# Performance work log

Measured on AMD Instinct MI355X. Metric: run time of the kernel, lower is better.

Reference implementation:

```python
import jax, jax.numpy as jnp
import numpy as np

NUM_POINTS = 72
GAMMA = 2.0
RADIUS = 15.0
W_CLS = 1.0
W_SIM = 3.0
LW_CLS = 2.0
LW_XYTL = 0.5
LW_LIOU = 2.0
K_MAX = 64
EPS = 1e-12  # F.normalize eps


def _normalize(v):
    # F.normalize over the flattened prior axis: v / max(||v||_2, eps)
    return v / jnp.maximum(jnp.linalg.norm(v), EPS)


def _liou_loss(pred, tgt):
    # pred: [..., P], tgt broadcastable; line IoU with radius, loss = 1 - iou
    lo = jnp.minimum(pred, tgt)
    hi = jnp.maximum(pred, tgt)
    ovr = (lo + RADIUS) - (hi - RADIUS)          # per-point overlap (may be < 0)
    union = (hi + RADIUS) - (lo - RADIUS)
    iou = jnp.sum(ovr, -1) / (jnp.sum(union, -1) + 1e-9)
    return 1.0 - iou


def _per_lane(feature, prior):
    # feature: [N, D] predictions for one image; prior: [D] one GT lane
    # ---- assignment cost ----
    logits = feature[:, :2]
    log_s = jax.nn.log_softmax(logits, axis=0)   # softmax over the N priors dim (dim=1 of [1,N,2])
    s = jnp.exp(log_s)
    focal_cost = jnp.sum(((1.0 - s) ** GAMMA) * log_s * prior[:2], axis=-1)  # [N]
    xy_cost = _normalize(jnp.sqrt(jnp.sum((feature[:, 3:5] - prior[3:5]) ** 2, -1)))  # [N]
    theta_cost = _normalize(feature[:, 5] - prior[5])                                  # [N]
    dis_cost = _normalize(jnp.sum(jnp.abs(feature[:, 6:] - prior[6:]), -1) / NUM_POINTS)  # [N]
    cost = W_SIM * (dis_cost * xy_cost * theta_cost) ** 2 + W_CLS * focal_cost
    # ---- dynamic top-k ----
    liou_all = _liou_loss(feature[:, 6:], prior[None, 6:])  # [N]
    k = jnp.clip(jnp.sum(liou_all).astype(jnp.int32), 1, K_MAX)
    _, idx = jax.lax.top_k(-cost, K_MAX)  # sorted ascending by cost; first k == topk(-cost, k)
    mask = (jnp.arange(K_MAX) < k).astype(feature.dtype)  # [K]
    kf = jnp.sum(mask)
    pf = feature[idx]  # [K, D] gathered predicted features
    # ---- xytl smooth-L1 on column-normalized concat([pred[:,2:6]; label[2:6]]) over valid rows ----
    rows = pf[:, 2:6]          # [K, 4]
    lab = prior[2:6]           # [4]
    colnorm = jnp.sqrt(jnp.sum((rows ** 2) * mask[:, None], 0) + lab ** 2)  # norm over the k+1 rows
    denom = jnp.maximum(colnorm, EPS)
    d = rows / denom - lab / denom  # [K, 4]
    ad = jnp.abs(d)
    sl1 = jnp.mean(jnp.where(ad < 1.0, 0.5 * d * d, ad - 0.5), -1)  # [K]
    sl1l = jnp.sum(sl1 * mask) / kf
    # ---- focal cls loss per assigned prior vs argmax of label cls ----
    tgt = jnp.argmax(prior[:2])
    lp = jax.nn.log_softmax(pf[:, :2], axis=-1)  # [K, 2]
    logpt = lp[:, tgt]
    pt = jnp.exp(logpt)
    fl_i = -((1.0 - pt) ** GAMMA) * logpt  # [K]
    fl = jnp.sum(fl_i * mask) / kf
    # ---- LIoU loss on assigned priors ----
    ll_i = _liou_loss(pf[:, 6:], prior[None, 6:])  # [K]
    ll = jnp.sum(ll_i * mask) / kf
    return sl1l, ll, fl


def setup_inputs() -> dict:
    key = jax.random.key(0)
    k1, k2 = jax.random.split(key)
    output = jax.random.normal(k1, (64, 1000, 78), dtype=jnp.float32)
    label = jax.random.normal(k2, (64, 16, 78), dtype=jnp.float32)
    return {"output": output, "label": label}


def reference(output, label):
    per_img = jax.vmap(_per_lane, in_axes=(None, 0))        # over lanes
    sl1l, ll, fl = jax.vmap(per_img, in_axes=(0, 0))(output, label)  # over batch
    sl1l = jnp.mean(sl1l)
    ll = jnp.mean(ll)
    fl = jnp.mean(fl)
    loss = (jnp.where(sl1l > 0, LW_XYTL * sl1l, 0.0)
            + jnp.where(ll > 0, LW_LIOU * ll, 0.0)
            + jnp.where(fl > 0, LW_CLS * fl, 0.0))
    return loss
```

## Files before the change

kernel.cpp:

```cpp
#include <hip/hip_runtime.h>
#include <math.h>

#define NROWS 1000
#define TWO_R_N 2160.0f
typedef unsigned int uint;
typedef unsigned long long ull;

#define OFF_RTS  1024000
#define OFF_INV  3072000
#define OFF_KK   3073024
#define OFF_OUT3 3074048

__device__ __forceinline__ float wsumf(float v){
#pragma unroll
  for(int o=32;o;o>>=1) v += __shfl_xor(v,o,64);
  return v;
}
__device__ __forceinline__ float wmaxf(float v){
#pragma unroll
  for(int o=32;o;o>>=1) v = fmaxf(v,__shfl_xor(v,o,64));
  return v;
}

__global__ __launch_bounds__(256,2) void clr_phase_a(const float* __restrict__ feat,
                                                     const float* __restrict__ lab,
                                                     float* __restrict__ ws)
{
  const int b  = blockIdx.x & 63;
  const int pg = blockIdx.x >> 6;
  const float* __restrict__ F  = feat + (size_t)b*NROWS*78;
  const float* __restrict__ PA = lab + ((size_t)b*16 + pg*2)*78;
  const float* __restrict__ PB = PA + 78;
  float2* __restrict__ C01  = (float2*)ws + (size_t)(b*8+pg)*NROWS;
  float2* __restrict__ RTS0 = (float2*)(ws + OFF_RTS) + (size_t)(b*16+pg*2)*NROWS;
  float2* __restrict__ RTS1 = RTS0 + NROWS;

  __shared__ float red[4][8];

  const int tid=threadIdx.x, wave=tid>>6, lane=tid&63;
  const int rloc16=lane>>2, q=lane&3;

  float pva[18], pvb[18];
#pragma unroll
  for(int s=0;s<18;++s){ pva[s]=PA[6+q+4*s]; pvb[s]=PB[6+q+4*s]; }
  const float2* PA2=(const float2*)PA;
  const float2* PB2=(const float2*)PB;
  const float2 a23=PA2[1], a45=PA2[2];
  const float2 b23=PB2[1], b45=PB2[2];

  float accR0=0.f,accT0=0.f,accD0=0.f,accL0=0.f;
  float accR1=0.f,accT1=0.f,accD1=0.f,accL1=0.f;

#pragma unroll 2
  for(int pass=0; pass<16; ++pass){
    const int rr = pass*64 + wave*16 + rloc16;
    if(rr < NROWS){
      const float* __restrict__ rp = F + rr*78;
      float part0=0.f, part1=0.f;
#pragma unroll
      for(int s=0;s<9;++s){
        const float x = rp[6+q+4*s];
        const float y = rp[6+q+4*(s+9)];
        part0 += fabsf(x - pva[s]);
        part0 += fabsf(y - pva[s+9]);
        part1 += fabsf(x - pvb[s]);
        part1 += fabsf(y - pvb[s+9]);
      }
      float s1a=part0+__shfl_xor(part0,1,64);
      float S0 = s1a +__shfl_xor(s1a, 2,64);
      float s1b=part1+__shfl_xor(part1,1,64);
      float S1 = s1b +__shfl_xor(s1b, 2,64);
      if(q==0){
        float d0=S0*(1.f/72.f); accD0+=d0*d0;
        accL0 += 1.f-(TWO_R_N-S0)/(TWO_R_N+S0+1e-9f);
        float d1=S1*(1.f/72.f); accD1+=d1*d1;
        accL1 += 1.f-(TWO_R_N-S1)/(TWO_R_N+S1+1e-9f);
      } else if(q==1){
        const float2* rp2=(const float2*)rp;
        const float2 c23=rp2[1], c45=rp2[2];
        float dr3=c23.y-a23.y, dr4=c45.x-a45.x, tt=c45.y-a45.y;
        float r2=dr3*dr3+dr4*dr4;
        RTS0[rr]=make_float2(sqrtf(r2)*tt, S0); accR0+=r2; accT0+=tt*tt;
        dr3=c23.y-b23.y; dr4=c45.x-b45.x; tt=c45.y-b45.y;
        r2=dr3*dr3+dr4*dr4;
        RTS1[rr]=make_float2(sqrtf(r2)*tt, S1); accR1+=r2; accT1+=tt*tt;
      } else if(q==2){
        const float2* rp2=(const float2*)rp;
        C01[rr]=rp2[0];
      }
    }
  }

  {
    float vR0=wsumf(accR0), vT0=wsumf(accT0), vD0=wsumf(accD0), vL0=wsumf(accL0);
    float vR1=wsumf(accR1), vT1=wsumf(accT1), vD1=wsumf(accD1), vL1=wsumf(accL1);
    if(lane==0){
      red[wave][0]=vR0; red[wave][1]=vT0; red[wave][2]=vD0; red[wave][3]=vL0;
      red[wave][4]=vR1; red[wave][5]=vT1; red[wave][6]=vD1; red[wave][7]=vL1;
    }
  }
  __syncthreads();
  if(wave>=2) return;
  const int w = wave;
  float R=0.f,T=0.f,D=0.f,L=0.f;
#pragma unroll
  for(int g=0;g<4;++g){
    R+=red[g][4*w]; T+=red[g][4*w+1]; D+=red[g][4*w+2]; L+=red[g][4*w+3];
  }
  float Nr=fmaxf(sqrtf(R),1e-12f), Nt=fmaxf(sqrtf(T),1e-12f), Nd=fmaxf(sqrtf(D),1e-12f);
  const float inv = 1.f/(Nr*Nt*Nd);
  int k=(int)L; if(k<1)k=1; if(k>64)k=64;
  if(lane==0){
    const int prior = b*16 + pg*2 + w;
    ws[OFF_INV + prior] = inv;
    ((int*)ws)[OFF_KK + prior] = k;
  }
}

__global__ __launch_bounds__(64,1) void clr_tail(const float* __restrict__ feat,
                                                 const float* __restrict__ lab,
                                                 float* __restrict__ ws)
{
  const int prior = blockIdx.x;
  const int b  = prior >> 4;
  const int pw = prior & 15;
  const int pair = b*8 + (pw>>1);
  const int lane = threadIdx.x;
  const float* __restrict__ F = feat + (size_t)b*NROWS*78;
  const float* __restrict__ P = lab + ((size_t)b*16 + pw)*78;
  const float2* __restrict__ C01 = (const float2*)ws + (size_t)pair*NROWS;
  const float2* __restrict__ RTS = (const float2*)(ws + OFF_RTS) + (size_t)prior*NROWS;
  const float inv = ws[OFF_INV + prior];
  const int   k   = ((const int*)ws)[OFF_KK + prior];

  __shared__ int selIdx[64];

  float2 c[16], rs[16];
#pragma unroll
  for(int t=0;t<16;++t){
    int i=t*64+lane; int ic = (i<NROWS)? i : (NROWS-1);
    c[t]=C01[ic]; rs[t]=RTS[ic];
  }

  const float2* P2=(const float2*)P;
  const float2 p01=P2[0], p23=P2[1], p45=P2[2];
  const float p0=p01.x, pp1=p01.y;

  float m0=-INFINITY, m1=-INFINITY;
#pragma unroll
  for(int t=0;t<16;++t){ int i=t*64+lane; if(i<NROWS){ m0=fmaxf(m0,c[t].x); m1=fmaxf(m1,c[t].y); } }
  m0=wmaxf(m0); m1=wmaxf(m1);
  float s0=0.f, s1=0.f;
#pragma unroll
  for(int t=0;t<16;++t){ int i=t*64+lane; if(i<NROWS){ s0+=__expf(c[t].x-m0); s1+=__expf(c[t].y-m1); } }
  s0=wsumf(s0); s1=wsumf(s1);
  const float lse0=m0+__logf(s0), lse1=m1+__logf(s1);

  uint key[16];
#pragma unroll
  for(int t=0;t<16;++t){
    int i=t*64+lane; uint kk=0xFFFFFFFFu;
    if(i<NROWS){
      float ls0=c[t].x-lse0, ls1=c[t].y-lse1;
      float e0=__expf(ls0), e1=__expf(ls1);
      float focal=(1.f-e0)*(1.f-e0)*ls0*p0 + (1.f-e1)*(1.f-e1)*ls1*pp1;
      float prod=rs[t].x*(rs[t].y*(1.f/72.f))*inv;
      float cost=3.f*prod*prod+focal;
      uint x=__float_as_uint(cost);
      kk=(x&0x80000000u)?~x:(x|0x80000000u);
    }
    key[t]=kk;
  }

  uint xx[16];
#pragma unroll
  for(int t=0;t<16;++t) xx[t]=key[t];
  uint pref=0u, r=(uint)k;
#pragma unroll
  for(int s=31;s>=0;--s){
    const uint bit=1u<<s;
    uint cnt=0u;
#pragma unroll
    for(int t=0;t<16;++t) cnt += (uint)__popcll(__ballot(xx[t]<bit));
    if(r>cnt){
      r-=cnt;
#pragma unroll
      for(int t=0;t<16;++t) xx[t]^=bit;
      pref|=bit;
    }
  }
  const uint T2=pref; uint need=r;

  const ull lmask=(1ull<<lane)-1ull;
  int base=0;
#pragma unroll
  for(int t=0;t<16;++t){
    bool lt = key[t]<T2;
    bool eq = key[t]==T2;
    ull meq=__ballot(eq);
    bool eqs = eq && ((uint)__popcll(meq&lmask)<need);
    uint teq=(uint)__popcll(meq);
    need -= (teq<need?teq:need);
    bool ssel = lt||eqs;
    ull ms=__ballot(ssel);
    if(ssel) selIdx[base+(int)__popcll(ms&lmask)] = t*64+lane;
    base += (int)__popcll(ms);
  }

  {
    bool act = lane<k;
    int idx = selIdx[act?lane:0];
    const float2* R2=(const float2*)(F+(size_t)idx*78);
    float2 g01=R2[0], g23=R2[1], g45=R2[2];
    float S = RTS[idx].y;
    float mk = act?1.f:0.f;
    float n2=wsumf(g23.x*g23.x*mk), n3=wsumf(g23.y*g23.y*mk);
    float n4=wsumf(g45.x*g45.x*mk), n5=wsumf(g45.y*g45.y*mk);
    float l2=p23.x, l3=p23.y, l4=p45.x, l5=p45.y;
    float de2=fmaxf(sqrtf(n2+l2*l2),1e-12f);
    float de3=fmaxf(sqrtf(n3+l3*l3),1e-12f);
    float de4=fmaxf(sqrtf(n4+l4*l4),1e-12f);
    float de5=fmaxf(sqrtf(n5+l5*l5),1e-12f);
    float d2=g23.x/de2-l2/de2, d3=g23.y/de3-l3/de3, d4=g45.x/de4-l4/de4, d5=g45.y/de5-l5/de5;
    auto h=[](float d){ float ad=fabsf(d); return ad<1.f ? 0.5f*d*d : ad-0.5f; };
    float sl1 = 0.25f*(h(d2)+h(d3)+h(d4)+h(d5));
    float mm=fmaxf(g01.x,g01.y);
    float lsee=mm+__logf(__expf(g01.x-mm)+__expf(g01.y-mm));
    float logpt=((pp1>p0)?g01.y:g01.x)-lsee;
    float pt=__expf(logpt);
    float fl=-(1.f-pt)*(1.f-pt)*logpt;
    float ll=1.f-(TWO_R_N-S)/(TWO_R_N+S+1e-9f);
    float ssl=wsumf(sl1*mk), sll=wsumf(ll*mk), sfl=wsumf(fl*mk);
    if(lane==0){
      float invk=1.f/(float)k;
      float* o = ws + OFF_OUT3 + (size_t)prior*3;
      o[0]=ssl*invk; o[1]=sll*invk; o[2]=sfl*invk;
    }
  }
}

__global__ __launch_bounds__(256) void clr_finalize(const float* __restrict__ ws,
                                                    float* __restrict__ out)
{
  const float* __restrict__ src = ws + OFF_OUT3;
  float a=0.f, bsum=0.f, c=0.f;
  for(int i=threadIdx.x;i<1024;i+=256){
    a    += src[i*3+0];
    bsum += src[i*3+1];
    c    += src[i*3+2];
  }
  a=wsumf(a); bsum=wsumf(bsum); c=wsumf(c);
  __shared__ float r[12];
  int wave=threadIdx.x>>6, lane=threadIdx.x&63;
  if(lane==0){ r[wave*3]=a; r[wave*3+1]=bsum; r[wave*3+2]=c; }
  __syncthreads();
  if(threadIdx.x==0){
    float sa=0,sb=0,sc=0;
    for(int w2=0;w2<4;w2++){sa+=r[w2*3];sb+=r[w2*3+1];sc+=r[w2*3+2];}
    float sl1l=sa*(1.f/1024.f), ll=sb*(1.f/1024.f), fl=sc*(1.f/1024.f);
    float loss = (sl1l>0.f ? 0.5f*sl1l : 0.f)
               + (ll  >0.f ? 2.0f*ll   : 0.f)
               + (fl  >0.f ? 2.0f*fl   : 0.f);
    out[0]=loss;
  }
}

extern "C" void kernel_launch(void* const* d_in, const int* in_sizes, int n_in,
                              void* d_out, int out_size, void* d_ws, size_t ws_size,
                              hipStream_t stream)
{
  const float* feat = (const float*)d_in[0];
  const float* lab  = (const float*)d_in[1];
  float* ws  = (float*)d_ws;
  float* out = (float*)d_out;
  hipLaunchKernelGGL(clr_phase_a, dim3(512),  dim3(256), 0, stream, feat, lab, ws);
  hipLaunchKernelGGL(clr_tail,    dim3(1024), dim3(64),  0, stream, feat, lab, ws);
  hipLaunchKernelGGL(clr_finalize,dim3(1),    dim3(256), 0, stream, ws, out);
}
```

Measured before the change: 104.2 us.

## Merge per-lane tail blocks into one 1024-thread block per image sharing logits

The tail kernel now launches one 1024-thread block per image instead of one 64-thread block per lane. The image's two logit columns are staged once in shared memory, and two waves compute the log-sum-exp for all sixteen lanes. This removes redundant global loads and softmax reductions that were repeated per lane. In exchange, the grid shrinks from 1024 to 64 blocks, so far fewer compute units are used and sixteen waves share each CU during the latency-bound radix select.

```diff
diff --git a/kernel.cpp b/kernel.cpp
--- a/kernel.cpp
+++ b/kernel.cpp
@@ -117,54 +117,56 @@
   }
 }
 
-__global__ __launch_bounds__(64,1) void clr_tail(const float* __restrict__ feat,
-                                                 const float* __restrict__ lab,
-                                                 float* __restrict__ ws)
-{
-  const int prior = blockIdx.x;
-  const int b  = prior >> 4;
-  const int pw = prior & 15;
-  const int pair = b*8 + (pw>>1);
-  const int lane = threadIdx.x;
+__global__ __launch_bounds__(1024,1) void clr_tail(const float* __restrict__ feat,
+                                                   const float* __restrict__ lab,
+                                                   float* __restrict__ ws)
+{
+  const int b = blockIdx.x;
+  const int tid=threadIdx.x, wave=tid>>6, lane=tid&63;
+  const int prior = b*16 + wave;
   const float* __restrict__ F = feat + (size_t)b*NROWS*78;
-  const float* __restrict__ P = lab + ((size_t)b*16 + pw)*78;
-  const float2* __restrict__ C01 = (const float2*)ws + (size_t)pair*NROWS;
+  const float* __restrict__ P = lab + (size_t)prior*78;
+  const float2* __restrict__ C01 = (const float2*)ws + (size_t)(b*8)*NROWS;
   const float2* __restrict__ RTS = (const float2*)(ws + OFF_RTS) + (size_t)prior*NROWS;
   const float inv = ws[OFF_INV + prior];
   const int   k   = ((const int*)ws)[OFF_KK + prior];
 
-  __shared__ int selIdx[64];
-
-  float2 c[16], rs[16];
-#pragma unroll
-  for(int t=0;t<16;++t){
-    int i=t*64+lane; int ic = (i<NROWS)? i : (NROWS-1);
-    c[t]=C01[ic]; rs[t]=RTS[ic];
-  }
+  __shared__ float sC0[NROWS], sC1[NROWS];
+  __shared__ float sLse[2];
+  __shared__ int   selIdx[16][64];
+
+  for(int i=tid;i<NROWS;i+=1024){ float2 v=C01[i]; sC0[i]=v.x; sC1[i]=v.y; }
+  __syncthreads();
+
+  if(wave<2){
+    const float* __restrict__ col = wave ? sC1 : sC0;
+    float m=-INFINITY;
+#pragma unroll
+    for(int t=0;t<16;++t){ int i=t*64+lane; if(i<NROWS) m=fmaxf(m,col[i]); }
+    m=wmaxf(m);
+    float ssum=0.f;
+#pragma unroll
+    for(int t=0;t<16;++t){ int i=t*64+lane; if(i<NROWS) ssum+=__expf(col[i]-m); }
+    ssum=wsumf(ssum);
+    if(lane==0) sLse[wave]=m+__logf(ssum);
+  }
+  __syncthreads();
+  const float lse0=sLse[0], lse1=sLse[1];
 
   const float2* P2=(const float2*)P;
   const float2 p01=P2[0], p23=P2[1], p45=P2[2];
   const float p0=p01.x, pp1=p01.y;
 
-  float m0=-INFINITY, m1=-INFINITY;
-#pragma unroll
-  for(int t=0;t<16;++t){ int i=t*64+lane; if(i<NROWS){ m0=fmaxf(m0,c[t].x); m1=fmaxf(m1,c[t].y); } }
-  m0=wmaxf(m0); m1=wmaxf(m1);
-  float s0=0.f, s1=0.f;
-#pragma unroll
-  for(int t=0;t<16;++t){ int i=t*64+lane; if(i<NROWS){ s0+=__expf(c[t].x-m0); s1+=__expf(c[t].y-m1); } }
-  s0=wsumf(s0); s1=wsumf(s1);
-  const float lse0=m0+__logf(s0), lse1=m1+__logf(s1);
-
   uint key[16];
 #pragma unroll
   for(int t=0;t<16;++t){
     int i=t*64+lane; uint kk=0xFFFFFFFFu;
     if(i<NROWS){
-      float ls0=c[t].x-lse0, ls1=c[t].y-lse1;
+      float2 rsv = RTS[i];
+      float ls0=sC0[i]-lse0, ls1=sC1[i]-lse1;
       float e0=__expf(ls0), e1=__expf(ls1);
       float focal=(1.f-e0)*(1.f-e0)*ls0*p0 + (1.f-e1)*(1.f-e1)*ls1*pp1;
-      float prod=rs[t].x*(rs[t].y*(1.f/72.f))*inv;
+      float prod=rsv.x*(rsv.y*(1.f/72.f))*inv;
       float cost=3.f*prod*prod+focal;
       uint x=__float_as_uint(cost);
       kk=(x&0x80000000u)?~x:(x|0x80000000u);
@@ -203,13 +205,13 @@
     need -= (teq<need?teq:need);
     bool ssel = lt||eqs;
     ull ms=__ballot(ssel);
-    if(ssel) selIdx[base+(int)__popcll(ms&lmask)] = t*64+lane;
+    if(ssel) selIdx[wave][base+(int)__popcll(ms&lmask)] = t*64+lane;
     base += (int)__popcll(ms);
   }
 
   {
     bool act = lane<k;
-    int idx = selIdx[act?lane:0];
+    int idx = selIdx[wave][act?lane:0];
     const float2* R2=(const float2*)(F+(size_t)idx*78);
     float2 g01=R2[0], g23=R2[1], g45=R2[2];
     float S = RTS[idx].y;
@@ -273,7 +275,7 @@
   const float* lab  = (const float*)d_in[1];
   float* ws  = (float*)d_ws;
   float* out = (float*)d_out;
-  hipLaunchKernelGGL(clr_phase_a, dim3(512),  dim3(256), 0, stream, feat, lab, ws);
-  hipLaunchKernelGGL(clr_tail,    dim3(1024), dim3(64),  0, stream, feat, lab, ws);
-  hipLaunchKernelGGL(clr_finalize,dim3(1),    dim3(256), 0, stream, ws, out);
-}
+  hipLaunchKernelGGL(clr_phase_a, dim3(512), dim3(256),  0, stream, feat, lab, ws);
+  hipLaunchKernelGGL(clr_tail,    dim3(64),  dim3(1024), 0, stream, feat, lab, ws);
+  hipLaunchKernelGGL(clr_finalize,dim3(1),   dim3(256),  0, stream, ws, out);
+}
```

Measured after the change: 107.4 us. +3.1%, slower.
